# Kernel optimization log

Measured on AMD Instinct MI355X. Metric: run time of the kernel, lower is better.

The kernel has to match this reference:

```python
import jax, jax.numpy as jnp
import numpy as np

N_ATOMS = 500_000
FEAT = 128
N_SUPPORT = 256
N_SPECIES = 4
N_STRUCT = 2000
ZETA = 2


def setup_inputs() -> dict:
    key = jax.random.key(0)
    k1, k2, k3, k4, k5 = jax.random.split(key, 5)
    power_spectrum = jax.random.normal(k1, (N_ATOMS, FEAT), dtype=jnp.float32)
    support_points = jax.random.normal(k2, (N_SPECIES, N_SUPPORT, FEAT), dtype=jnp.float32)
    # CosineKernel asserts support points are unit-norm
    support_points = support_points / jnp.linalg.norm(support_points, axis=-1, keepdims=True)
    weights = jax.random.normal(k3, (N_SPECIES, N_SUPPORT), dtype=jnp.float32)
    all_species = jax.random.randint(k4, (N_ATOMS,), 0, N_SPECIES, dtype=jnp.int64)
    # structures_slices in the original are contiguous slices -> sorted structure ids
    structure_ids = jnp.sort(jax.random.randint(k5, (N_ATOMS,), 0, N_STRUCT, dtype=jnp.int64))
    return {
        "power_spectrum": power_spectrum,
        "support_points": support_points,
        "weights": weights,
        "all_species": all_species,
        "structure_ids": structure_ids,
        "n_structures": N_STRUCT,
    }


def reference(power_spectrum, support_points, weights, all_species, structure_ids, n_structures):
    # Normalize each environment (CosineKernel normalization)
    norm = jnp.linalg.norm(power_spectrum, axis=1, keepdims=True)
    nps = power_spectrum / norm  # [N, D]

    # Per-atom scalar energy contribution; species loop is over a tiny fixed set.
    per_atom = jnp.zeros((power_spectrum.shape[0],), dtype=power_spectrum.dtype)
    for s in range(support_points.shape[0]):
        k_nm = (nps @ support_points[s].T) ** ZETA  # [N, M]
        contrib = k_nm @ weights[s]  # [N]
        per_atom = per_atom + jnp.where(all_species == s, contrib, jnp.zeros_like(contrib))

    # Sum per-atom contributions within each structure (replaces the structure loop)
    energy = jax.ops.segment_sum(per_atom, structure_ids, num_segments=n_structures)
    return energy[:, None]  # [n_structures, 1]
```

## Files before the change

kernel.cpp:

```cpp
#include <hip/hip_runtime.h>

#define KF 128
#define NSUP 256
#define NSPEC 4
#define GRID 256
#define BLOCK 512

typedef __bf16 bf16x8 __attribute__((ext_vector_type(8)));
typedef float  f32x4  __attribute__((ext_vector_type(4)));


__global__ void k_buildG(const float* __restrict__ sup, const float* __restrict__ w,
                         __bf16* __restrict__ gfrag) {
    const int t = blockIdx.x * blockDim.x + threadIdx.x;
    if (t >= NSPEC * 8 * 4 * 64) return;
    const int lane = t & 63;
    const int kk   = (t >> 6) & 3;
    const int ct   = (t >> 8) & 7;
    const int s    = t >> 11;
    const int i    = lane & 15;
    const int c    = (ct >> 1) * 32 + (i >> 2) * 8 + (ct & 1) * 4 + (i & 3);
    const int k0   = kk * 32 + (lane >> 4) * 8;
    const float* S = sup + (size_t)s * NSUP * KF;
    const float* W = w + s * NSUP;
    float a0 = 0.f, a1 = 0.f, a2 = 0.f, a3 = 0.f, a4 = 0.f, a5 = 0.f, a6 = 0.f, a7 = 0.f;
    for (int m = 0; m < NSUP; ++m) {
        const float wc = W[m] * S[m * KF + c];
        const float4 ka = *(const float4*)(S + m * KF + k0);
        const float4 kb = *(const float4*)(S + m * KF + k0 + 4);
        a0 += wc * ka.x; a1 += wc * ka.y; a2 += wc * ka.z; a3 += wc * ka.w;
        a4 += wc * kb.x; a5 += wc * kb.y; a6 += wc * kb.z; a7 += wc * kb.w;
    }
    bf16x8 o;
    o[0] = (__bf16)a0; o[1] = (__bf16)a1; o[2] = (__bf16)a2; o[3] = (__bf16)a3;
    o[4] = (__bf16)a4; o[5] = (__bf16)a5; o[6] = (__bf16)a6; o[7] = (__bf16)a7;
    *(bf16x8*)(gfrag + (size_t)t * 8) = o;
}


__device__ __forceinline__ bf16x8 pack8(float4 a, float4 b) {
    bf16x8 o;
    o[0] = (__bf16)a.x; o[1] = (__bf16)a.y; o[2] = (__bf16)a.z; o[3] = (__bf16)a.w;
    o[4] = (__bf16)b.x; o[5] = (__bf16)b.y; o[6] = (__bf16)b.z; o[7] = (__bf16)b.w;
    return o;
}

__device__ __forceinline__ float sq4(float4 a) {
    return a.x * a.x + a.y * a.y + a.z * a.z + a.w * a.w;
}

#define LOAD_SET(BASE, OFF, SPC, SID, V, NN, X0, X1, X2, X3)              \
    {                                                                     \
        int _a = (BASE) + (OFF) + r;                                      \
        V = _a < n;                                                       \
        int _ra = V ? _a : 0;                                             \
        SPC = V ? species[_ra] : -1;                                      \
        SID = V ? sids[_ra] : 0;                                          \
        const float* _p = ps + (size_t)_ra * KF + g * 8;                  \
        float4 _q0 = V ? *(const float4*)(_p +   0) : z4;                 \
        float4 _q1 = V ? *(const float4*)(_p +   4) : z4;                 \
        float4 _q2 = V ? *(const float4*)(_p +  32) : z4;                 \
        float4 _q3 = V ? *(const float4*)(_p +  36) : z4;                 \
        float4 _q4 = V ? *(const float4*)(_p +  64) : z4;                 \
        float4 _q5 = V ? *(const float4*)(_p +  68) : z4;                 \
        float4 _q6 = V ? *(const float4*)(_p +  96) : z4;                 \
        float4 _q7 = V ? *(const float4*)(_p + 100) : z4;                 \
        NN = sq4(_q0) + sq4(_q1) + sq4(_q2) + sq4(_q3)                    \
           + sq4(_q4) + sq4(_q5) + sq4(_q6) + sq4(_q7);                   \
        NN += __shfl_xor(NN, 16);                                         \
        NN += __shfl_xor(NN, 32);                                         \
        X0 = pack8(_q0, _q1); X1 = pack8(_q2, _q3);                       \
        X2 = pack8(_q4, _q5); X3 = pack8(_q6, _q7);                       \
    }

#define GSTEP2(CT, XA, XB)                                                      \
    {                                                                           \
        const __bf16* gq = gp + (CT) * 2048;                                    \
        const bf16x8 g0 = *(const bf16x8*)(gq);                                 \
        const bf16x8 g1 = *(const bf16x8*)(gq + 512);                           \
        const bf16x8 g2 = *(const bf16x8*)(gq + 1024);                          \
        const bf16x8 g3 = *(const bf16x8*)(gq + 1536);                          \
        f32x4 aA = (f32x4){0.f, 0.f, 0.f, 0.f};                                 \
        f32x4 aB = (f32x4){0.f, 0.f, 0.f, 0.f};                                 \
        aA = __builtin_amdgcn_mfma_f32_16x16x32_bf16(g0, cA0, aA, 0, 0, 0);     \
        aB = __builtin_amdgcn_mfma_f32_16x16x32_bf16(g0, cB0, aB, 0, 0, 0);     \
        aA = __builtin_amdgcn_mfma_f32_16x16x32_bf16(g1, cA1, aA, 0, 0, 0);     \
        aB = __builtin_amdgcn_mfma_f32_16x16x32_bf16(g1, cB1, aB, 0, 0, 0);     \
        aA = __builtin_amdgcn_mfma_f32_16x16x32_bf16(g2, cA2, aA, 0, 0, 0);     \
        aB = __builtin_amdgcn_mfma_f32_16x16x32_bf16(g2, cB2, aB, 0, 0, 0);     \
        aA = __builtin_amdgcn_mfma_f32_16x16x32_bf16(g3, cA3, aA, 0, 0, 0);     \
        aB = __builtin_amdgcn_mfma_f32_16x16x32_bf16(g3, cB3, aB, 0, 0, 0);     \
        const int _o = ((CT) & 1) * 4;                                          \
        esA += aA[0] * (float)XA[_o + 0] + aA[1] * (float)XA[_o + 1]            \
             + aA[2] * (float)XA[_o + 2] + aA[3] * (float)XA[_o + 3];           \
        esB += aB[0] * (float)XB[_o + 0] + aB[1] * (float)XB[_o + 1]            \
             + aB[2] * (float)XB[_o + 2] + aB[3] * (float)XB[_o + 3];           \
    }


__global__ __launch_bounds__(BLOCK, 1) void k_main(
    const float* __restrict__ ps,
    const __bf16* __restrict__ gfrag,
    const int* __restrict__ species,
    const int* __restrict__ sids,
    float* __restrict__ out,
    int n)
{
    __shared__ __align__(16) __bf16 Glds[NSPEC * 128 * 128];

    for (int f = threadIdx.x; f < 8192; f += BLOCK)
        ((int4*)Glds)[f] = ((const int4*)gfrag)[f];
    __syncthreads();

    const int lane = threadIdx.x & 63;
    const int r = lane & 15, g = lane >> 4;
    const int wid = blockIdx.x * (BLOCK / 64) + (threadIdx.x >> 6);
    const int gs = GRID * (BLOCK / 64);
    const int ntiles = (n + 31) / 32;

    const float4 z4 = make_float4(0.f, 0.f, 0.f, 0.f);

    for (int t = wid; t < ntiles; t += gs) {
        int spcA, sidA, spcB, sidB;
        bool vA, vB;
        float nnA, nnB;
        bf16x8 cA0, cA1, cA2, cA3, cB0, cB1, cB2, cB3;

        LOAD_SET(t * 32, 0,  spcA, sidA, vA, nnA, cA0, cA1, cA2, cA3)
        LOAD_SET(t * 32, 16, spcB, sidB, vB, nnB, cB0, cB1, cB2, cB3)

        float eA = 0.f, eB = 0.f;
        #pragma unroll 1
        for (int s = 0; s < NSPEC; ++s) {
            const __bf16* gp = Glds + s * 16384 + lane * 8;
            float esA = 0.f, esB = 0.f;
            GSTEP2(0, cA0, cB0)
            GSTEP2(1, cA0, cB0)
            __builtin_amdgcn_sched_barrier(0);
            GSTEP2(2, cA1, cB1)
            GSTEP2(3, cA1, cB1)
            __builtin_amdgcn_sched_barrier(0);
            GSTEP2(4, cA2, cB2)
            GSTEP2(5, cA2, cB2)
            __builtin_amdgcn_sched_barrier(0);
            GSTEP2(6, cA3, cB3)
            GSTEP2(7, cA3, cB3)
            eA += (spcA == s) ? esA : 0.f;
            eB += (spcB == s) ? esB : 0.f;
        }

        float uA = (nnA > 0.f) ? eA / nnA : 0.f;
        float uB = (nnB > 0.f) ? eB / nnB : 0.f;

        const int s0 = __shfl(sidA, 0);
        const bool uni = __all(sidA == s0) && __all(sidB == s0);
        if (uni) {
            float tot = uA + uB;
            tot += __shfl_xor(tot, 1);  tot += __shfl_xor(tot, 2);
            tot += __shfl_xor(tot, 4);  tot += __shfl_xor(tot, 8);
            tot += __shfl_xor(tot, 16); tot += __shfl_xor(tot, 32);
            if (lane == 0 && tot != 0.f) atomicAdd(&out[s0], tot);
        } else {
            uA += __shfl_xor(uA, 16); uA += __shfl_xor(uA, 32);
            uB += __shfl_xor(uB, 16); uB += __shfl_xor(uB, 32);
            if (g == 0) {
                if (vA) atomicAdd(&out[sidA], uA);
                if (vB) atomicAdd(&out[sidB], uB);
            }
        }
    }
}


__global__ void k_fallback(const float* __restrict__ ps, const float* __restrict__ support,
                           const float* __restrict__ weights, const int* __restrict__ species,
                           const int* __restrict__ struct_ids, float* __restrict__ out, int n)
{
    int gw = (blockIdx.x * blockDim.x + threadIdx.x) >> 6;
    int lane = threadIdx.x & 63;
    int nw = (gridDim.x * blockDim.x) >> 6;
    for (int atom = gw; atom < n; atom += nw) {
        const float* row = ps + (size_t)atom * KF;
        float x0 = row[lane], x1 = row[lane + 64];
        float nsum = x0 * x0 + x1 * x1;
        for (int o = 32; o; o >>= 1) nsum += __shfl_xor(nsum, o);
        float iv2 = 1.0f / nsum;
        int s = species[atom];
        const float* sup = support + (size_t)s * NSUP * KF;
        const float* w = weights + (size_t)s * NSUP;
        float e = 0.f;
        for (int mm = 0; mm < 4; ++mm) {
            int m = lane + mm * 64;
            const float* srow = sup + (size_t)m * KF;
            float d = 0.f;
            for (int k = 0; k < KF; ++k) d += row[k] * srow[k];
            e += d * d * w[m];
        }
        for (int o = 32; o; o >>= 1) e += __shfl_xor(e, o);
        if (lane == 0) atomicAdd(&out[struct_ids[atom]], e * iv2);
    }
}


extern "C" void kernel_launch(void* const* d_in, const int* in_sizes, int n_in,
                              void* d_out, int out_size, void* d_ws, size_t ws_size,
                              hipStream_t stream)
{
    const float* ps       = (const float*)d_in[0];
    const float* support  = (const float*)d_in[1];
    const float* weights  = (const float*)d_in[2];
    const int*   species  = (const int*)d_in[3];
    const int*   sids     = (const int*)d_in[4];
    float* out = (float*)d_out;
    const int n = in_sizes[0] / KF;

    hipMemsetAsync(d_out, 0, (size_t)out_size * sizeof(float), stream);

    const size_t gbytes = (size_t)NSPEC * 8 * 4 * 64 * 8 * sizeof(__bf16);
    if (ws_size < gbytes) {
        k_fallback<<<2048, 256, 0, stream>>>(ps, support, weights, species, sids, out, n);
        return;
    }

    __bf16* gfrag = (__bf16*)d_ws;
    k_buildG<<<(NSPEC * 8 * 4 * 64 + 255) / 256, 256, 0, stream>>>(support, weights, gfrag);
    k_main<<<GRID, BLOCK, 0, stream>>>(ps, gfrag, species, sids, out, n);
}
```

Measured before the change: 194.9 us.

## Bucket atoms by species so each block computes only its species kernel

Adds a counting pass and a scatter pass that build a per-species index list of atoms. Each block of the main kernel then handles one species and loads only that species' G matrix into LDS, which removes the 4x redundant MFMA work of evaluating every species for every atom. The cost is two extra launches, gathered (indirect) reads of rows that break coalescing locality, and weaker structure-id uniformity per wave, so more atomics fall on the slow per-atom path. Grid and block shape also change, to 1024 blocks of 256 threads.

After: 295.0 us. +51.3%, slower.

```diff
diff --git a/kernel.cpp b/kernel.cpp
--- a/kernel.cpp
+++ b/kernel.cpp
@@ -3,11 +3,44 @@
 #define KF 128
 #define NSUP 256
 #define NSPEC 4
-#define GRID 256
-#define BLOCK 512
+#define GRID 1024
+#define BLOCK 256
 
 typedef __bf16 bf16x8 __attribute__((ext_vector_type(8)));
 typedef float  f32x4  __attribute__((ext_vector_type(4)));
+
+
+__global__ void k_count(const int* __restrict__ sp, int n, int* __restrict__ counts) {
+    __shared__ int h[NSPEC];
+    if (threadIdx.x < NSPEC) h[threadIdx.x] = 0;
+    __syncthreads();
+    for (int i = blockIdx.x * blockDim.x + threadIdx.x; i < n; i += gridDim.x * blockDim.x)
+        atomicAdd(&h[sp[i]], 1);
+    __syncthreads();
+    if (threadIdx.x < NSPEC) atomicAdd(&counts[threadIdx.x], h[threadIdx.x]);
+}
+
+__global__ void k_scatter(const int* __restrict__ sp, int n,
+                          const int* __restrict__ counts, int* __restrict__ cursors,
+                          int* __restrict__ order) {
+    __shared__ int lh[NSPEC];
+    __shared__ int basep[NSPEC];
+    if (threadIdx.x < NSPEC) lh[threadIdx.x] = 0;
+    __syncthreads();
+    int i = blockIdx.x * blockDim.x + threadIdx.x;
+    int s = (i < n) ? sp[i] : -1;
+    int local = 0;
+    if (s >= 0) local = atomicAdd(&lh[s], 1);
+    __syncthreads();
+    if (threadIdx.x < NSPEC) {
+        int q = threadIdx.x;
+        int off = 0;
+        for (int u = 0; u < q; ++u) off += counts[u];
+        basep[q] = off + atomicAdd(&cursors[q], lh[q]);
+    }
+    __syncthreads();
+    if (s >= 0) order[basep[s] + local] = i;
+}
 
 
 __global__ void k_buildG(const float* __restrict__ sup, const float* __restrict__ w,
@@ -49,12 +82,11 @@
     return a.x * a.x + a.y * a.y + a.z * a.z + a.w * a.w;
 }
 
-#define LOAD_SET(BASE, OFF, SPC, SID, V, NN, X0, X1, X2, X3)              \
+#define LOAD_SET(LOC, SID, V, NN, X0, X1, X2, X3)                         \
     {                                                                     \
-        int _a = (BASE) + (OFF) + r;                                      \
-        V = _a < n;                                                       \
-        int _ra = V ? _a : 0;                                             \
-        SPC = V ? species[_ra] : -1;                                      \
+        int _l = (LOC) + r;                                               \
+        V = _l < cnt;                                                     \
+        int _ra = V ? order[off + _l] : 0;                                \
         SID = V ? sids[_ra] : 0;                                          \
         const float* _p = ps + (size_t)_ra * KF + g * 8;                  \
         float4 _q0 = V ? *(const float4*)(_p +   0) : z4;                 \
@@ -101,56 +133,60 @@
 __global__ __launch_bounds__(BLOCK, 1) void k_main(
     const float* __restrict__ ps,
     const __bf16* __restrict__ gfrag,
-    const int* __restrict__ species,
+    const int* __restrict__ counts,
+    const int* __restrict__ order,
     const int* __restrict__ sids,
     float* __restrict__ out,
     int n)
 {
-    __shared__ __align__(16) __bf16 Glds[NSPEC * 128 * 128];
-
-    for (int f = threadIdx.x; f < 8192; f += BLOCK)
-        ((int4*)Glds)[f] = ((const int4*)gfrag)[f];
-    __syncthreads();
+    __shared__ __align__(16) __bf16 Glds[128 * 128];
+
+    const int spec = blockIdx.x & 3;
+    {
+        const int4* src = (const int4*)(gfrag + (size_t)spec * 16384);
+        for (int f = threadIdx.x; f < 2048; f += BLOCK)
+            ((int4*)Glds)[f] = src[f];
+    }
+    __syncthreads();
+
+    int off = 0;
+    #pragma unroll
+    for (int q = 0; q < NSPEC; ++q) { if (q < spec) off += counts[q]; }
+    const int cnt = counts[spec];
 
     const int lane = threadIdx.x & 63;
     const int r = lane & 15, g = lane >> 4;
-    const int wid = blockIdx.x * (BLOCK / 64) + (threadIdx.x >> 6);
-    const int gs = GRID * (BLOCK / 64);
-    const int ntiles = (n + 31) / 32;
+    const int wsp = (blockIdx.x >> 2) * (BLOCK / 64) + (threadIdx.x >> 6);
+    const int gs = (GRID / 4) * (BLOCK / 64);
+    const int ntiles = (cnt + 31) / 32;
 
     const float4 z4 = make_float4(0.f, 0.f, 0.f, 0.f);
 
-    for (int t = wid; t < ntiles; t += gs) {
-        int spcA, sidA, spcB, sidB;
+    for (int t = wsp; t < ntiles; t += gs) {
+        int sidA, sidB;
         bool vA, vB;
         float nnA, nnB;
         bf16x8 cA0, cA1, cA2, cA3, cB0, cB1, cB2, cB3;
 
-        LOAD_SET(t * 32, 0,  spcA, sidA, vA, nnA, cA0, cA1, cA2, cA3)
-        LOAD_SET(t * 32, 16, spcB, sidB, vB, nnB, cB0, cB1, cB2, cB3)
-
-        float eA = 0.f, eB = 0.f;
-        #pragma unroll 1
-        for (int s = 0; s < NSPEC; ++s) {
-            const __bf16* gp = Glds + s * 16384 + lane * 8;
-            float esA = 0.f, esB = 0.f;
-            GSTEP2(0, cA0, cB0)
-            GSTEP2(1, cA0, cB0)
-            __builtin_amdgcn_sched_barrier(0);
-            GSTEP2(2, cA1, cB1)
-            GSTEP2(3, cA1, cB1)
-            __builtin_amdgcn_sched_barrier(0);
-            GSTEP2(4, cA2, cB2)
-            GSTEP2(5, cA2, cB2)
-            __builtin_amdgcn_sched_barrier(0);
-            GSTEP2(6, cA3, cB3)
-            GSTEP2(7, cA3, cB3)
-            eA += (spcA == s) ? esA : 0.f;
-            eB += (spcB == s) ? esB : 0.f;
-        }
-
-        float uA = (nnA > 0.f) ? eA / nnA : 0.f;
-        float uB = (nnB > 0.f) ? eB / nnB : 0.f;
+        LOAD_SET(t * 32,      sidA, vA, nnA, cA0, cA1, cA2, cA3)
+        LOAD_SET(t * 32 + 16, sidB, vB, nnB, cB0, cB1, cB2, cB3)
+
+        const __bf16* gp = Glds + lane * 8;
+        float esA = 0.f, esB = 0.f;
+        GSTEP2(0, cA0, cB0)
+        GSTEP2(1, cA0, cB0)
+        __builtin_amdgcn_sched_barrier(0);
+        GSTEP2(2, cA1, cB1)
+        GSTEP2(3, cA1, cB1)
+        __builtin_amdgcn_sched_barrier(0);
+        GSTEP2(4, cA2, cB2)
+        GSTEP2(5, cA2, cB2)
+        __builtin_amdgcn_sched_barrier(0);
+        GSTEP2(6, cA3, cB3)
+        GSTEP2(7, cA3, cB3)
+
+        float uA = (vA && nnA > 0.f) ? esA / nnA : 0.f;
+        float uB = (vB && nnB > 0.f) ? esB / nnB : 0.f;
 
         const int s0 = __shfl(sidA, 0);
         const bool uni = __all(sidA == s0) && __all(sidB == s0);
@@ -217,12 +253,24 @@
     hipMemsetAsync(d_out, 0, (size_t)out_size * sizeof(float), stream);
 
     const size_t gbytes = (size_t)NSPEC * 8 * 4 * 64 * 8 * sizeof(__bf16);
-    if (ws_size < gbytes) {
+    size_t order_end = 64 + (size_t)n * sizeof(int);
+    size_t gfrag_off = (order_end + 15) & ~(size_t)15;
+    const size_t need = gfrag_off + gbytes;
+    if (ws_size < need) {
         k_fallback<<<2048, 256, 0, stream>>>(ps, support, weights, species, sids, out, n);
         return;
     }
 
-    __bf16* gfrag = (__bf16*)d_ws;
+    int* ws      = (int*)d_ws;
+    int* counts  = ws;
+    int* cursors = ws + 8;
+    int* order   = ws + 16;
+    __bf16* gfrag = (__bf16*)((char*)d_ws + gfrag_off);
+
+    hipMemsetAsync(ws, 0, 64, stream);
+    k_count<<<512, 256, 0, stream>>>(species, n, counts);
+    k_scatter<<<(n + 255) / 256, 256, 0, stream>>>(species, n, counts, cursors, order);
     k_buildG<<<(NSPEC * 8 * 4 * 64 + 255) / 256, 256, 0, stream>>>(support, weights, gfrag);
-    k_main<<<GRID, BLOCK, 0, stream>>>(ps, gfrag, species, sids, out, n);
-}
+
+    k_main<<<GRID, BLOCK, 0, stream>>>(ps, gfrag, counts, order, sids, out, n);
+}
```
